# Kernel tuning notes

Hardware: AMD Instinct MI355X
Metric: run time of the kernel (lower is better)

Reference implementation:

```python
import jax, jax.numpy as jnp
import numpy as np

N = 262144            # inflated nodes (atoms + edge-nodes)
E = 4 * 1024 * 1024   # directed edges
D = 8                 # node_feature_dim
TD = 1                # time_dim
H = 32                # hidden_channels
L = 4                 # num_layers
BN_EPS = 1e-5


def setup_inputs() -> dict:
    key = jax.random.key(0)
    ks = jax.random.split(key, 12)
    s = 0.1  # small init scale
    return {
        "x": jax.random.normal(ks[0], (N, D), jnp.float32),
        "t": jax.random.uniform(ks[1], (1,), jnp.float32),
        "edge_index": jax.random.randint(ks[2], (2, E), 0, N, jnp.int32),
        "node_mask": jax.random.randint(ks[3], (N,), 0, 2) > 0,
        "edge_mask": jax.random.randint(ks[4], (N,), 0, 2) > 0,
        "ond": 5,  # original_node_feature_dim
        "oed": 4,  # original_edge_feature_dim
        # GINConv MLP params: layer 0 has in=D+TD, layers 1..3 have in=H
        "W1_first": jax.random.normal(ks[5], (D + TD, H), jnp.float32) * s,
        "b1_first": jnp.zeros((H,), jnp.float32),
        "W2_first": jax.random.normal(ks[6], (H, H), jnp.float32) * s,
        "b2_first": jnp.zeros((H,), jnp.float32),
        "W1_rest": jax.random.normal(ks[7], (L - 1, H, H), jnp.float32) * s,
        "b1_rest": jnp.zeros((L - 1, H), jnp.float32),
        "W2_rest": jax.random.normal(ks[8], (L - 1, H, H), jnp.float32) * s,
        "b2_rest": jnp.zeros((L - 1, H), jnp.float32),
        "eps": jnp.zeros((L,), jnp.float32),           # train_eps=True, init 0
        "bn_gamma": jnp.ones((L, H), jnp.float32),
        "bn_beta": jnp.zeros((L, H), jnp.float32),
        "lin_W": jax.random.normal(ks[9], (L * H, D), jnp.float32) * s,
        "lin_b": jnp.zeros((D,), jnp.float32),
    }


def _gin_forward(x, t, W1_first, b1_first, W2_first, b2_first,
                 W1_rest, b1_rest, W2_rest, b2_rest, eps, bn_gamma, bn_beta,
                 lin_W, lin_b, edge_index, node_mask, edge_mask, ond, oed):
    src = edge_index[0]
    dst = edge_index[1]
    n = x.shape[0]
    # x_in = cat(x, t*ones)
    tcol = jnp.full((n, 1), t[0], x.dtype)
    h = jnp.concatenate([x, tcol], axis=1)  # [N, D+TD]
    xs = []
    for l in range(L):
        # GINConv: (1+eps)*x_i + sum_{j->i} x_j, then 2-layer MLP
        agg = jax.ops.segment_sum(h[src], dst, num_segments=n)  # scatter-add
        z = (1.0 + eps[l]) * h + agg
        W1 = W1_first if l == 0 else W1_rest[l - 1]
        b1 = b1_first if l == 0 else b1_rest[l - 1]
        W2 = W2_first if l == 0 else W2_rest[l - 1]
        b2 = b2_first if l == 0 else b2_rest[l - 1]
        z = jax.nn.relu(z @ W1 + b1) @ W2 + b2  # [N, H]
        # BatchNorm (training-mode batch stats), then ReLU; dropout=eval->id
        mu = jnp.mean(z, axis=0)
        var = jnp.var(z, axis=0)
        z = (z - mu) * jax.lax.rsqrt(var + BN_EPS) * bn_gamma[l] + bn_beta[l]
        h = jax.nn.relu(z)
        xs.append(h)
    # JK 'cat' + final Linear(L*H -> D)
    new_x = jnp.concatenate(xs, axis=1) @ lin_W + lin_b  # [N, D]
    # masked feature write-back: x[mask, 1:dim+1] = new_x[mask, 1:dim+1]
    cols = jnp.arange(x.shape[1])
    ncols = (cols >= 1) & (cols < ond + 1)
    ecols = (cols >= 1) & (cols < oed + 1)
    out = jnp.where(node_mask[:, None] & ncols[None, :], new_x, x)
    out = jnp.where(edge_mask[:, None] & ecols[None, :], new_x, out)
    return out


def reference(x, t, edge_index, node_mask, edge_mask, ond, oed,
              W1_first, b1_first, W2_first, b2_first,
              W1_rest, b1_rest, W2_rest, b2_rest,
              eps, bn_gamma, bn_beta, lin_W, lin_b):
    return _gin_forward(x, t, W1_first, b1_first, W2_first, b2_first,
                        W1_rest, b1_rest, W2_rest, b2_rest,
                        eps, bn_gamma, bn_beta, lin_W, lin_b,
                        edge_index, node_mask, edge_mask, ond, oed)
```

## Files before the change

kernel.cpp:

```cpp
#include <hip/hip_runtime.h>
#include <cstdint>

#define NN 262144
#define EE 4194304
#define CAP 64
#define NB 512
#define BSZ 512
#define NSH 8
#define SCAP 1280
#define EPB 8192
#define SLICES 64

typedef __attribute__((ext_vector_type(8))) short bf16x8;
typedef __attribute__((ext_vector_type(4))) float f32x4;
#define MFMA16 __builtin_amdgcn_mfma_f32_16x16x32_bf16

__device__ inline float bf2f(unsigned short u) {
  union { unsigned int i; float f; } v; v.i = ((unsigned int)u) << 16; return v.f;
}
__device__ inline unsigned short f2bf(float f) {
  union { float f; unsigned int i; } v; v.f = f;
  unsigned int r = v.i + 0x7FFF + ((v.i >> 16) & 1);
  return (unsigned short)(r >> 16);
}
__device__ inline float blo(unsigned int u) {
  union { unsigned int i; float f; } v; v.i = u << 16; return v.f;
}
__device__ inline float bhi(unsigned int u) {
  union { unsigned int i; float f; } v; v.i = u & 0xFFFF0000u; return v.f;
}

__global__ void k_curinit(int* __restrict__ cur) {
  int i = blockIdx.x * 256 + threadIdx.x;
  if (i < NSH * NB) cur[i] = i * SCAP;
}

__global__ void __launch_bounds__(256, 1)
k_bin(const int* __restrict__ ei, int* __restrict__ cur, int* __restrict__ pair) {
  __shared__ int hist[NB];
  __shared__ int off[NB];
  __shared__ int gbase[NB];
  __shared__ int psum[256];
  __shared__ int ebuf[EPB];
  const int tid = threadIdx.x, blk = blockIdx.x, sh = blk & (NSH - 1);
  const int* esrc = ei + (size_t)blk * EPB;
  const int* edst = ei + EE + (size_t)blk * EPB;

  for (int k = tid; k < NB; k += 256) hist[k] = 0;
  __syncthreads();
  for (int j = tid; j < EPB / 4; j += 256) {
    int4 d4 = ((const int4*)edst)[j];
    atomicAdd(&hist[d4.x >> 9], 1);
    atomicAdd(&hist[d4.y >> 9], 1);
    atomicAdd(&hist[d4.z >> 9], 1);
    atomicAdd(&hist[d4.w >> 9], 1);
  }
  __syncthreads();
  int a0 = hist[2 * tid], a1 = hist[2 * tid + 1];
  int ps = a0 + a1;
  psum[tid] = ps;
  __syncthreads();
  for (int d = 1; d < 256; d <<= 1) {
    int v = (tid >= d) ? psum[tid - d] : 0;
    __syncthreads();
    psum[tid] += v;
    __syncthreads();
  }
  int excl = psum[tid] - ps;
  off[2 * tid] = excl;
  off[2 * tid + 1] = excl + a0;
  __syncthreads();
  for (int b = tid; b < NB; b += 256) {
    int n = hist[b];
    int ci = sh * NB + b;
    gbase[b] = n ? atomicAdd(&cur[ci], n) : ci * SCAP;
  }
  __syncthreads();
  for (int k = tid; k < NB; k += 256) hist[k] = off[k];
  __syncthreads();
  for (int j = tid; j < EPB / 4; j += 256) {
    int4 s4 = ((const int4*)esrc)[j];
    int4 d4 = ((const int4*)edst)[j];
    int dd[4] = {d4.x, d4.y, d4.z, d4.w};
    int ss[4] = {s4.x, s4.y, s4.z, s4.w};
#pragma unroll
    for (int u = 0; u < 4; ++u) {
      int bin = dd[u] >> 9, dl = dd[u] & (BSZ - 1);
      int p = atomicAdd(&hist[bin], 1);
      ebuf[p] = ss[u] | (dl << 18);
    }
  }
  __syncthreads();
  for (int b = tid; b < NB; b += 256) {
    int st = off[b];
    int n = hist[b] - st;
    int ci = sh * NB + b;
    int gb = gbase[b];
    int lim = ci * SCAP + SCAP;
    if (gb + n > lim) n = (lim > gb) ? (lim - gb) : 0;
    for (int k = 0; k < n; ++k) pair[gb + k] = ebuf[st + k];
  }
}

__global__ void k_expand(const int* __restrict__ cur, const int* __restrict__ pair,
                         int* __restrict__ slot, int* __restrict__ deg) {
  __shared__ int cbin[BSZ];
  int tid = threadIdx.x;
  int bin = blockIdx.x;
  for (int k = tid; k < BSZ; k += 512) cbin[k] = 0;
  __syncthreads();
  for (int s = 0; s < NSH; ++s) {
    int ci = s * NB + bin, base = ci * SCAP;
    int cnt = min(cur[ci] - base, SCAP);
    for (int k = tid; k < cnt; k += 512) {
      int p = pair[base + k];
      int src = p & 0x3FFFF, dl = p >> 18;
      int pos = atomicAdd(&cbin[dl], 1);
      if (pos < CAP)
        slot[((size_t)bin * BSZ + dl) * CAP + pos] = src;
    }
  }
  __syncthreads();
  for (int k = tid; k < BSZ; k += 512) {
    int cnt = min(cbin[k], CAP);
    int cntp = (cnt + 15) & ~15;
    int self = bin * BSZ + k;
    for (int p = cnt; p < cntp; ++p)
      slot[((size_t)bin * BSZ + k) * CAP + p] = self;
    deg[bin * BSZ + k] = cnt;
  }
}

__global__ void k_layer0(const float* __restrict__ x, const float* __restrict__ t,
                         const int* __restrict__ slot, const int* __restrict__ deg,
                         const float* __restrict__ W1, const float* __restrict__ b1,
                         const float* __restrict__ W2, const float* __restrict__ b2,
                         const float* __restrict__ epsv,
                         unsigned short* __restrict__ zb,
                         float* __restrict__ ssum, float* __restrict__ ssq) {
  __shared__ __align__(16) unsigned short wt1h[32 * 40], wt1l[32 * 40];
  __shared__ __align__(16) unsigned short wt2h[32 * 40], wt2l[32 * 40];
  __shared__ __align__(16) unsigned short insh[16 * 40], insl[16 * 40];
  __shared__ __align__(16) unsigned short z1h[16 * 40], z1l[16 * 40];
  __shared__ float aggs[8][8];
  int tid = threadIdx.x;
  int c = tid & 31, g = tid >> 5;
  size_t base = (size_t)blockIdx.x * 16;

  for (int k = tid; k < 32 * 40; k += 256) { wt1h[k] = 0; wt1l[k] = 0; }
  for (int k = tid; k < 16 * 40; k += 256) { insh[k] = 0; insl[k] = 0; }
  __syncthreads();
  if (tid < 72) {
    float4 wv = ((const float4*)W1)[tid];
    int k = tid >> 3, n4 = (tid & 7) * 4;
    float v[4] = {wv.x, wv.y, wv.z, wv.w};
#pragma unroll
    for (int j = 0; j < 4; ++j) {
      unsigned short h = f2bf(v[j]);
      wt1h[(n4 + j) * 40 + k] = h;
      wt1l[(n4 + j) * 40 + k] = f2bf(v[j] - bf2f(h));
    }
  }
  {
    float4 wv = ((const float4*)W2)[tid];
    int k = tid >> 3, n4 = (tid & 7) * 4;
    float v[4] = {wv.x, wv.y, wv.z, wv.w};
#pragma unroll
    for (int j = 0; j < 4; ++j) {
      unsigned short h = f2bf(v[j]);
      wt2h[(n4 + j) * 40 + k] = h;
      wt2l[(n4 + j) * 40 + k] = f2bf(v[j] - bf2f(h));
    }
  }

  float t0 = t[0];
  float epsl = epsv[0];

  for (int half = 0; half < 2; ++half) {
    int row = g + 8 * half;
    size_t i = base + row;
    int cnt = deg[i];
    int cntp = (cnt + 15) & ~15;
    const int* sl = slot + i * CAP;
    int sv = sl[c];
    float xself = (c < 8) ? x[i * 8 + c] : 0.f;

    int q = c & 1, e = c >> 1;
    float4 agg4 = {0.f, 0.f, 0.f, 0.f};
    int kmax = min(cntp, 32);
    for (int k = 0; k < kmax; k += 16) {
      int s = __shfl(sv, k + e, 32);
      float4 v = ((const float4*)x)[(size_t)s * 2 + q];
      agg4.x += v.x; agg4.y += v.y; agg4.z += v.z; agg4.w += v.w;
    }
    if (cntp > 32) {
      int sv2 = sl[32 + c];
      for (int k = 32; k < cntp; k += 16) {
        int s = __shfl(sv2, (k - 32) + e, 32);
        float4 v = ((const float4*)x)[(size_t)s * 2 + q];
        agg4.x += v.x; agg4.y += v.y; agg4.z += v.z; agg4.w += v.w;
      }
    }
#pragma unroll
    for (int off = 2; off < 32; off <<= 1) {
      agg4.x += __shfl_xor(agg4.x, off, 32);
      agg4.y += __shfl_xor(agg4.y, off, 32);
      agg4.z += __shfl_xor(agg4.z, off, 32);
      agg4.w += __shfl_xor(agg4.w, off, 32);
    }
    if (c < 2) ((float4*)aggs[g])[q] = agg4;
    __syncthreads();

    float pad = (float)(cntp - cnt);
    if (c < 9) {
      float inval = (c < 8) ? ((1.f + epsl) * xself + aggs[g][c] - pad * xself)
                            : ((1.f + epsl) * t0 + (float)cnt * t0);
      unsigned short h = f2bf(inval);
      insh[row * 40 + c] = h;
      insl[row * 40 + c] = f2bf(inval - bf2f(h));
    }
    __syncthreads();
  }

  int w = tid >> 6, lane = tid & 63;
  int nsel = (w & 1) * 16 + (lane & 15);
  int kb = (lane >> 4) * 8;
  if (w < 2) {
    bf16x8 ah = *(const bf16x8*)&insh[(lane & 15) * 40 + kb];
    bf16x8 al = *(const bf16x8*)&insl[(lane & 15) * 40 + kb];
    bf16x8 bh = *(const bf16x8*)&wt1h[nsel * 40 + kb];
    bf16x8 bl = *(const bf16x8*)&wt1l[nsel * 40 + kb];
    f32x4 c1 = {0.f, 0.f, 0.f, 0.f};
    c1 = MFMA16(ah, bh, c1, 0, 0, 0);
    c1 = MFMA16(al, bh, c1, 0, 0, 0);
    c1 = MFMA16(ah, bl, c1, 0, 0, 0);
    float bias1 = b1[nsel];
#pragma unroll
    for (int r = 0; r < 4; ++r) {
      int rr = (lane >> 4) * 4 + r;
      float z = fmaxf(c1[r] + bias1, 0.f);
      unsigned short h = f2bf(z);
      z1h[rr * 40 + nsel] = h;
      z1l[rr * 40 + nsel] = f2bf(z - bf2f(h));
    }
  }
  __syncthreads();
  if (w < 2) {
    bf16x8 ah = *(const bf16x8*)&z1h[(lane & 15) * 40 + kb];
    bf16x8 al = *(const bf16x8*)&z1l[(lane & 15) * 40 + kb];
    bf16x8 bh = *(const bf16x8*)&wt2h[nsel * 40 + kb];
    bf16x8 bl = *(const bf16x8*)&wt2l[nsel * 40 + kb];
    f32x4 c2 = {0.f, 0.f, 0.f, 0.f};
    c2 = MFMA16(ah, bh, c2, 0, 0, 0);
    c2 = MFMA16(al, bh, c2, 0, 0, 0);
    c2 = MFMA16(ah, bl, c2, 0, 0, 0);
    float bias2 = b2[nsel];
    float s1 = 0.f, s2 = 0.f;
#pragma unroll
    for (int r = 0; r < 4; ++r) {
      int rr = (lane >> 4) * 4 + r;
      float z = c2[r] + bias2;
      zb[(base + rr) * 32 + nsel] = f2bf(z);
      s1 += z; s2 += z * z;
    }
    s1 += __shfl_xor(s1, 16, 64); s2 += __shfl_xor(s2, 16, 64);
    s1 += __shfl_xor(s1, 32, 64); s2 += __shfl_xor(s2, 32, 64);
    if ((lane >> 4) == 0) {
      int slice = blockIdx.x & (SLICES - 1);
      atomicAdd(&ssum[slice * 32 + nsel], s1);
      atomicAdd(&ssq[slice * 32 + nsel], s2);
    }
  }
}

__global__ void k_bnapply(const unsigned short* __restrict__ zb,
                          const float* __restrict__ ssum, const float* __restrict__ ssq,
                          const float* __restrict__ gamma, const float* __restrict__ beta,
                          const float* __restrict__ linW,
                          unsigned short* __restrict__ hb,
                          float* __restrict__ out_acc, int first_acc) {
  __shared__ float linWs[256];
  __shared__ float scs[32], shs[32];
  int tid = threadIdx.x;
  for (int k = tid; k < 256; k += 256) linWs[k] = linW[k];
  if (tid < 32) {
    float s1 = 0.f, s2 = 0.f;
    for (int s = 0; s < SLICES; ++s) { s1 += ssum[s * 32 + tid]; s2 += ssq[s * 32 + tid]; }
    float mu = s1 * (1.f / NN);
    float var = s2 * (1.f / NN) - mu * mu;
    float sc = gamma[tid] * rsqrtf(var + 1e-5f);
    scs[tid] = sc;
    shs[tid] = beta[tid] - mu * sc;
  }
  int r = tid & 3;
  size_t n = (size_t)blockIdx.x * 64 + (tid >> 2);
  uint4 u = ((const uint4*)zb)[n * 4 + r];
  __syncthreads();

  float h[8];
#pragma unroll
  for (int j = 0; j < 8; ++j) {
    unsigned int w = (j < 2) ? u.x : (j < 4) ? u.y : (j < 6) ? u.z : u.w;
    float zv = (j & 1) ? bhi(w) : blo(w);
    h[j] = fmaxf(zv * scs[8 * r + j] + shs[8 * r + j], 0.f);
  }
  uint4 o;
  o.x = (unsigned int)f2bf(h[0]) | ((unsigned int)f2bf(h[1]) << 16);
  o.y = (unsigned int)f2bf(h[2]) | ((unsigned int)f2bf(h[3]) << 16);
  o.z = (unsigned int)f2bf(h[4]) | ((unsigned int)f2bf(h[5]) << 16);
  o.w = (unsigned int)f2bf(h[6]) | ((unsigned int)f2bf(h[7]) << 16);
  ((uint4*)hb)[n * 4 + r] = o;

  float jk[8];
#pragma unroll
  for (int d = 0; d < 8; ++d) {
    float a = 0.f;
#pragma unroll
    for (int j = 0; j < 8; ++j) a += h[j] * linWs[(8 * r + j) * 8 + d];
    jk[d] = a;
  }
#pragma unroll
  for (int off = 1; off <= 2; off <<= 1)
#pragma unroll
    for (int d = 0; d < 8; ++d) jk[d] += __shfl_xor(jk[d], off, 64);
  if (r == 0) {
    float4 a0 = {jk[0], jk[1], jk[2], jk[3]};
    float4 a1 = {jk[4], jk[5], jk[6], jk[7]};
    if (!first_acc) {
      float4 p0 = ((const float4*)out_acc)[n * 2];
      float4 p1 = ((const float4*)out_acc)[n * 2 + 1];
      a0.x += p0.x; a0.y += p0.y; a0.z += p0.z; a0.w += p0.w;
      a1.x += p1.x; a1.y += p1.y; a1.z += p1.z; a1.w += p1.w;
    }
    ((float4*)out_acc)[n * 2] = a0;
    ((float4*)out_acc)[n * 2 + 1] = a1;
  }
}

__global__ void k_layerN(const unsigned short* __restrict__ hb,
                         const int* __restrict__ slot, const int* __restrict__ deg,
                         const float* __restrict__ W1, const float* __restrict__ b1,
                         const float* __restrict__ W2, const float* __restrict__ b2,
                         const float* __restrict__ epsv, int l,
                         unsigned short* __restrict__ zbo,
                         float* __restrict__ ssum, float* __restrict__ ssq) {
  __shared__ __align__(16) unsigned short wt1h[32 * 40], wt1l[32 * 40];
  __shared__ __align__(16) unsigned short wt2h[32 * 40], wt2l[32 * 40];
  __shared__ __align__(16) unsigned short insh[16 * 40], insl[16 * 40];
  __shared__ __align__(16) unsigned short z1h[16 * 40], z1l[16 * 40];
  __shared__ float aggs[8][32];
  int tid = threadIdx.x;
  int c = tid & 31, g = tid >> 5;
  size_t base = (size_t)blockIdx.x * 16;

  {
    float4 w1v = ((const float4*)W1)[tid];
    float4 w2v = ((const float4*)W2)[tid];
    int k = tid >> 3, n4 = (tid & 7) * 4;
    float v1[4] = {w1v.x, w1v.y, w1v.z, w1v.w};
    float v2[4] = {w2v.x, w2v.y, w2v.z, w2v.w};
#pragma unroll
    for (int j = 0; j < 4; ++j) {
      unsigned short h1 = f2bf(v1[j]);
      wt1h[(n4 + j) * 40 + k] = h1;
      wt1l[(n4 + j) * 40 + k] = f2bf(v1[j] - bf2f(h1));
      unsigned short h2 = f2bf(v2[j]);
      wt2h[(n4 + j) * 40 + k] = h2;
      wt2l[(n4 + j) * 40 + k] = f2bf(v2[j] - bf2f(h2));
    }
  }

  float epsl = epsv[l];

  for (int half = 0; half < 2; ++half) {
    int row = g + 8 * half;
    size_t i = base + row;
    int cnt = deg[i];
    int cntp = (cnt + 15) & ~15;
    const int* sl = slot + i * CAP;
    int sv = sl[c];
    float hself = bf2f(hb[i * 32 + c]);

    int q = c & 7, sub = c >> 3;
    const ushort4* h4 = (const ushort4*)hb;
    float4 agg4 = {0.f, 0.f, 0.f, 0.f};
    int kmax = min(cntp, 32);
    for (int k = 0; k < kmax; k += 16) {
      int sa = __shfl(sv, k + sub, 32);
      int sb = __shfl(sv, k + 4 + sub, 32);
      int sc_ = __shfl(sv, k + 8 + sub, 32);
      int sd = __shfl(sv, k + 12 + sub, 32);
      ushort4 ua = h4[(size_t)sa * 8 + q];
      ushort4 ub = h4[(size_t)sb * 8 + q];
      ushort4 uc = h4[(size_t)sc_ * 8 + q];
      ushort4 ud = h4[(size_t)sd * 8 + q];
      agg4.x += bf2f(ua.x) + bf2f(ub.x) + bf2f(uc.x) + bf2f(ud.x);
      agg4.y += bf2f(ua.y) + bf2f(ub.y) + bf2f(uc.y) + bf2f(ud.y);
      agg4.z += bf2f(ua.z) + bf2f(ub.z) + bf2f(uc.z) + bf2f(ud.z);
      agg4.w += bf2f(ua.w) + bf2f(ub.w) + bf2f(uc.w) + bf2f(ud.w);
    }
    if (cntp > 32) {
      int sv2 = sl[32 + c];
      for (int k = 32; k < cntp; k += 16) {
        int kk = k - 32;
        int sa = __shfl(sv2, kk + sub, 32);
        int sb = __shfl(sv2, kk + 4 + sub, 32);
        int sc_ = __shfl(sv2, kk + 8 + sub, 32);
        int sd = __shfl(sv2, kk + 12 + sub, 32);
        ushort4 ua = h4[(size_t)sa * 8 + q];
        ushort4 ub = h4[(size_t)sb * 8 + q];
        ushort4 uc = h4[(size_t)sc_ * 8 + q];
        ushort4 ud = h4[(size_t)sd * 8 + q];
        agg4.x += bf2f(ua.x) + bf2f(ub.x) + bf2f(uc.x) + bf2f(ud.x);
        agg4.y += bf2f(ua.y) + bf2f(ub.y) + bf2f(uc.y) + bf2f(ud.y);
        agg4.z += bf2f(ua.z) + bf2f(ub.z) + bf2f(uc.z) + bf2f(ud.z);
        agg4.w += bf2f(ua.w) + bf2f(ub.w) + bf2f(uc.w) + bf2f(ud.w);
      }
    }
    agg4.x += __shfl_xor(agg4.x, 8, 32);
    agg4.y += __shfl_xor(agg4.y, 8, 32);
    agg4.z += __shfl_xor(agg4.z, 8, 32);
    agg4.w += __shfl_xor(agg4.w, 8, 32);
    agg4.x += __shfl_xor(agg4.x, 16, 32);
    agg4.y += __shfl_xor(agg4.y, 16, 32);
    agg4.z += __shfl_xor(agg4.z, 16, 32);
    agg4.w += __shfl_xor(agg4.w, 16, 32);
    if (c < 8) ((float4*)aggs[g])[q] = agg4;
    __syncthreads();

    float pad = (float)(cntp - cnt);
    float inval = (1.f + epsl - pad) * hself + aggs[g][c];
    unsigned short h = f2bf(inval);
    insh[row * 40 + c] = h;
    insl[row * 40 + c] = f2bf(inval - bf2f(h));
    __syncthreads();
  }

  int w = tid >> 6, lane = tid & 63;
  int nsel = (w & 1) * 16 + (lane & 15);
  int kb = (lane >> 4) * 8;
  if (w < 2) {
    bf16x8 ah = *(const bf16x8*)&insh[(lane & 15) * 40 + kb];
    bf16x8 al = *(const bf16x8*)&insl[(lane & 15) * 40 + kb];
    bf16x8 bh = *(const bf16x8*)&wt1h[nsel * 40 + kb];
    bf16x8 bl = *(const bf16x8*)&wt1l[nsel * 40 + kb];
    f32x4 c1 = {0.f, 0.f, 0.f, 0.f};
    c1 = MFMA16(ah, bh, c1, 0, 0, 0);
    c1 = MFMA16(al, bh, c1, 0, 0, 0);
    c1 = MFMA16(ah, bl, c1, 0, 0, 0);
    float bias1 = b1[nsel];
#pragma unroll
    for (int r = 0; r < 4; ++r) {
      int rr = (lane >> 4) * 4 + r;
      float z = fmaxf(c1[r] + bias1, 0.f);
      unsigned short h = f2bf(z);
      z1h[rr * 40 + nsel] = h;
      z1l[rr * 40 + nsel] = f2bf(z - bf2f(h));
    }
  }
  __syncthreads();
  if (w < 2) {
    bf16x8 ah = *(const bf16x8*)&z1h[(lane & 15) * 40 + kb];
    bf16x8 al = *(const bf16x8*)&z1l[(lane & 15) * 40 + kb];
    bf16x8 bh = *(const bf16x8*)&wt2h[nsel * 40 + kb];
    bf16x8 bl = *(const bf16x8*)&wt2l[nsel * 40 + kb];
    f32x4 c2 = {0.f, 0.f, 0.f, 0.f};
    c2 = MFMA16(ah, bh, c2, 0, 0, 0);
    c2 = MFMA16(al, bh, c2, 0, 0, 0);
    c2 = MFMA16(ah, bl, c2, 0, 0, 0);
    float bias2 = b2[nsel];
    float s1 = 0.f, s2 = 0.f;
#pragma unroll
    for (int r = 0; r < 4; ++r) {
      int rr = (lane >> 4) * 4 + r;
      float z = c2[r] + bias2;
      zbo[(base + rr) * 32 + nsel] = f2bf(z);
      s1 += z; s2 += z * z;
    }
    s1 += __shfl_xor(s1, 16, 64); s2 += __shfl_xor(s2, 16, 64);
    s1 += __shfl_xor(s1, 32, 64); s2 += __shfl_xor(s2, 32, 64);
    if ((lane >> 4) == 0) {
      int slice = blockIdx.x & (SLICES - 1);
      atomicAdd(&ssum[slice * 32 + nsel], s1);
      atomicAdd(&ssq[slice * 32 + nsel], s2);
    }
  }
}

__global__ void k_final(const unsigned short* __restrict__ z3,
                        const float* __restrict__ ssum, const float* __restrict__ ssq,
                        const float* __restrict__ gamma, const float* __restrict__ beta,
                        const float* __restrict__ linW3, const float* __restrict__ lin_b,
                        const float* __restrict__ out_acc, const float* __restrict__ x,
                        const int* __restrict__ nm, const int* __restrict__ em,
                        const int* __restrict__ ondp, const int* __restrict__ oedp,
                        float* __restrict__ out) {
  __shared__ float linWs[256];
  __shared__ float scs[32], shs[32];
  int tid = threadIdx.x;
  for (int k = tid; k < 256; k += 256) linWs[k] = linW3[k];
  if (tid < 32) {
    float s1 = 0.f, s2 = 0.f;
    for (int s = 0; s < SLICES; ++s) { s1 += ssum[s * 32 + tid]; s2 += ssq[s * 32 + tid]; }
    float mu = s1 * (1.f / NN);
    float var = s2 * (1.f / NN) - mu * mu;
    float sc = gamma[tid] * rsqrtf(var + 1e-5f);
    scs[tid] = sc;
    shs[tid] = beta[tid] - mu * sc;
  }
  int r = tid & 3;
  size_t n = (size_t)blockIdx.x * 64 + (tid >> 2);
  uint4 u = ((const uint4*)z3)[n * 4 + r];
  __syncthreads();

  float h[8];
#pragma unroll
  for (int j = 0; j < 8; ++j) {
    unsigned int w = (j < 2) ? u.x : (j < 4) ? u.y : (j < 6) ? u.z : u.w;
    float zv = (j & 1) ? bhi(w) : blo(w);
    h[j] = fmaxf(zv * scs[8 * r + j] + shs[8 * r + j], 0.f);
  }
  float jk[8];
#pragma unroll
  for (int d = 0; d < 8; ++d) {
    float a = 0.f;
#pragma unroll
    for (int j = 0; j < 8; ++j) a += h[j] * linWs[(8 * r + j) * 8 + d];
    jk[d] = a;
  }
#pragma unroll
  for (int off = 1; off <= 2; off <<= 1)
#pragma unroll
    for (int d = 0; d < 8; ++d) jk[d] += __shfl_xor(jk[d], off, 64);
  if (r == 0) {
    float4 p0 = ((const float4*)out_acc)[n * 2];
    float4 p1 = ((const float4*)out_acc)[n * 2 + 1];
    float4 x0 = ((const float4*)x)[n * 2];
    float4 x1 = ((const float4*)x)[n * 2 + 1];
    float res[8] = {jk[0] + p0.x + lin_b[0], jk[1] + p0.y + lin_b[1],
                    jk[2] + p0.z + lin_b[2], jk[3] + p0.w + lin_b[3],
                    jk[4] + p1.x + lin_b[4], jk[5] + p1.y + lin_b[5],
                    jk[6] + p1.z + lin_b[6], jk[7] + p1.w + lin_b[7]};
    float xs[8] = {x0.x, x0.y, x0.z, x0.w, x1.x, x1.y, x1.z, x1.w};
    int ond = ondp[0], oed = oedp[0];
    bool nmv = nm[n] != 0, emv = em[n] != 0;
    float o[8];
#pragma unroll
    for (int d = 0; d < 8; ++d) {
      bool w = (d >= 1) && ((nmv && d < ond + 1) || (emv && d < oed + 1));
      o[d] = w ? res[d] : xs[d];
    }
    ((float4*)out)[n * 2]     = make_float4(o[0], o[1], o[2], o[3]);
    ((float4*)out)[n * 2 + 1] = make_float4(o[4], o[5], o[6], o[7]);
  }
}

extern "C" void kernel_launch(void* const* d_in, const int* in_sizes, int n_in,
                              void* d_out, int out_size, void* d_ws, size_t ws_size,
                              hipStream_t stream) {
  const float* x        = (const float*)d_in[0];
  const float* t        = (const float*)d_in[1];
  const int*   ei       = (const int*)d_in[2];
  const int*   node_mask= (const int*)d_in[3];
  const int*   edge_mask= (const int*)d_in[4];
  const int*   ondp     = (const int*)d_in[5];
  const int*   oedp     = (const int*)d_in[6];
  const float* W1_first = (const float*)d_in[7];
  const float* b1_first = (const float*)d_in[8];
  const float* W2_first = (const float*)d_in[9];
  const float* b2_first = (const float*)d_in[10];
  const float* W1_rest  = (const float*)d_in[11];
  const float* b1_rest  = (const float*)d_in[12];
  const float* W2_rest  = (const float*)d_in[13];
  const float* b2_rest  = (const float*)d_in[14];
  const float* epsv     = (const float*)d_in[15];
  const float* bn_gamma = (const float*)d_in[16];
  const float* bn_beta  = (const float*)d_in[17];
  const float* lin_W    = (const float*)d_in[18];
  const float* lin_b    = (const float*)d_in[19];
  float* out = (float*)d_out;

  char* ws = (char*)d_ws;
  size_t off = 0;
  int*   slot    = (int*)(ws + off);   off += (size_t)NN * CAP * 4;
  int*   pair    = (int*)(ws + off);   off += (size_t)NSH * NB * SCAP * 4;
  int*   cur     = (int*)(ws + off);   off += (size_t)NSH * NB * 4;
  int*   deg     = (int*)(ws + off);   off += (size_t)NN * 4;
  unsigned short* zb = (unsigned short*)(ws + off); off += (size_t)NN * 32 * 2;
  unsigned short* hb = (unsigned short*)(ws + off); off += (size_t)NN * 32 * 2;
  float* out_acc = (float*)(ws + off); off += (size_t)NN * 8 * 4;
  float* stats   = (float*)(ws + off); off += (size_t)4 * 2 * SLICES * 32 * 4;
  (void)ws_size; (void)in_sizes; (void)n_in; (void)out_size;

  hipMemsetAsync(stats, 0, (size_t)4 * 2 * SLICES * 32 * 4, stream);
  k_curinit<<<(NSH * NB + 255) / 256, 256, 0, stream>>>(cur);
  k_bin<<<EE / EPB, 256, 0, stream>>>(ei, cur, pair);
  k_expand<<<NB, 512, 0, stream>>>(cur, pair, slot, deg);

  {
    float* ssum = stats;
    float* ssq  = ssum + SLICES * 32;
    k_layer0<<<NN / 16, 256, 0, stream>>>(x, t, slot, deg, W1_first, b1_first,
                                          W2_first, b2_first, epsv, zb, ssum, ssq);
    k_bnapply<<<NN / 64, 256, 0, stream>>>(zb, ssum, ssq, bn_gamma, bn_beta,
                                           lin_W, hb, out_acc, 1);
  }
  for (int l = 1; l < 4; ++l) {
    const float* W1 = W1_rest + (size_t)(l - 1) * 32 * 32;
    const float* b1 = b1_rest + (size_t)(l - 1) * 32;
    const float* W2 = W2_rest + (size_t)(l - 1) * 32 * 32;
    const float* b2 = b2_rest + (size_t)(l - 1) * 32;
    float* ssum = stats + (size_t)l * 2 * SLICES * 32;
    float* ssq  = ssum + SLICES * 32;
    k_layerN<<<NN / 16, 256, 0, stream>>>(hb, slot, deg, W1, b1, W2, b2,
                                          epsv, l, zb, ssum, ssq);
    if (l < 3)
      k_bnapply<<<NN / 64, 256, 0, stream>>>(zb, ssum, ssq, bn_gamma + l * 32,
                                             bn_beta + l * 32,
                                             lin_W + (size_t)l * 32 * 8,
                                             hb, out_acc, 0);
  }
  k_final<<<NN / 64, 256, 0, stream>>>(zb, stats + 3 * 2 * SLICES * 32,
                                       stats + 3 * 2 * SLICES * 32 + SLICES * 32,
                                       bn_gamma + 96, bn_beta + 96,
                                       lin_W + 3 * 32 * 8, lin_b, out_acc, x,
                                       node_mask, edge_mask, ondp, oedp, out);
}
```

Measured before the change: 523.0 us.

## Precompute swizzled split-bf16 weight images, pad neighbors to 8, interleave two-row gathers

```diff
diff --git a/kernel.cpp b/kernel.cpp
--- a/kernel.cpp
+++ b/kernel.cpp
@@ -13,6 +13,7 @@
 
 typedef __attribute__((ext_vector_type(8))) short bf16x8;
 typedef __attribute__((ext_vector_type(4))) float f32x4;
+typedef __attribute__((ext_vector_type(2))) float f32x2;
 #define MFMA16 __builtin_amdgcn_mfma_f32_16x16x32_bf16
 
 __device__ inline float bf2f(unsigned short u) {
@@ -29,10 +30,46 @@
 __device__ inline float bhi(unsigned int u) {
   union { unsigned int i; float f; } v; v.i = u & 0xFFFF0000u; return v.f;
 }
-
-__global__ void k_curinit(int* __restrict__ cur) {
-  int i = blockIdx.x * 256 + threadIdx.x;
-  if (i < NSH * NB) cur[i] = i * SCAP;
+__device__ inline f32x2 bfpair(unsigned int u) {
+  union { unsigned int i; float f; } lo, hi;
+  lo.i = u << 16; hi.i = u & 0xFFFF0000u;
+  return (f32x2){lo.f, hi.f};
+}
+
+__global__ void k_prep(int* __restrict__ cur,
+                       const float* __restrict__ W1f, const float* __restrict__ W2f,
+                       const float* __restrict__ W1r, const float* __restrict__ W2r,
+                       unsigned short* __restrict__ wimg) {
+  int tid = threadIdx.x;
+  if (blockIdx.x < 16) {
+    int i = blockIdx.x * 256 + tid;
+    if (i < NSH * NB) cur[i] = i * SCAP;
+    return;
+  }
+  for (int k = tid; k < 4 * 4 * 1280; k += 256) wimg[k] = 0;
+  __syncthreads();
+  for (int l = 0; l < 4; ++l) {
+    const float* W1 = (l == 0) ? W1f : W1r + (size_t)(l - 1) * 1024;
+    const float* W2 = (l == 0) ? W2f : W2r + (size_t)(l - 1) * 1024;
+    int kdim = (l == 0) ? 9 : 32;
+    unsigned short* bm = wimg + (size_t)l * 5120;
+    for (int e = tid; e < kdim * 32; e += 256) {
+      int k = e >> 5, n = e & 31;
+      float v = W1[e];
+      unsigned short h = f2bf(v);
+      int idx = n * 40 + (k ^ (n & 8));
+      bm[idx] = h;
+      bm[1280 + idx] = f2bf(v - bf2f(h));
+    }
+    for (int e = tid; e < 1024; e += 256) {
+      int k = e >> 5, n = e & 31;
+      float v = W2[e];
+      unsigned short h = f2bf(v);
+      int idx = n * 40 + (k ^ (n & 8));
+      bm[2560 + idx] = h;
+      bm[3840 + idx] = f2bf(v - bf2f(h));
+    }
+  }
 }
 
 __global__ void __launch_bounds__(256, 1)
@@ -123,7 +160,7 @@
   __syncthreads();
   for (int k = tid; k < BSZ; k += 512) {
     int cnt = min(cbin[k], CAP);
-    int cntp = (cnt + 15) & ~15;
+    int cntp = (cnt + 7) & ~7;
     int self = bin * BSZ + k;
     for (int p = cnt; p < cntp; ++p)
       slot[((size_t)bin * BSZ + k) * CAP + p] = self;
@@ -133,103 +170,112 @@
 
 __global__ void k_layer0(const float* __restrict__ x, const float* __restrict__ t,
                          const int* __restrict__ slot, const int* __restrict__ deg,
-                         const float* __restrict__ W1, const float* __restrict__ b1,
-                         const float* __restrict__ W2, const float* __restrict__ b2,
+                         const unsigned short* __restrict__ wimg,
+                         const float* __restrict__ b1, const float* __restrict__ b2,
                          const float* __restrict__ epsv,
                          unsigned short* __restrict__ zb,
                          float* __restrict__ ssum, float* __restrict__ ssq) {
-  __shared__ __align__(16) unsigned short wt1h[32 * 40], wt1l[32 * 40];
-  __shared__ __align__(16) unsigned short wt2h[32 * 40], wt2l[32 * 40];
-  __shared__ __align__(16) unsigned short insh[16 * 40], insl[16 * 40];
-  __shared__ __align__(16) unsigned short z1h[16 * 40], z1l[16 * 40];
-  __shared__ float aggs[8][8];
+  __shared__ __align__(16) unsigned short wbuf[5120];
+  __shared__ __align__(16) unsigned short insh[640], insl[640], z1h[640], z1l[640];
+  __shared__ float aggs0[2][8][8];
   int tid = threadIdx.x;
   int c = tid & 31, g = tid >> 5;
   size_t base = (size_t)blockIdx.x * 16;
 
-  for (int k = tid; k < 32 * 40; k += 256) { wt1h[k] = 0; wt1l[k] = 0; }
-  for (int k = tid; k < 16 * 40; k += 256) { insh[k] = 0; insl[k] = 0; }
-  __syncthreads();
-  if (tid < 72) {
-    float4 wv = ((const float4*)W1)[tid];
-    int k = tid >> 3, n4 = (tid & 7) * 4;
-    float v[4] = {wv.x, wv.y, wv.z, wv.w};
-#pragma unroll
-    for (int j = 0; j < 4; ++j) {
-      unsigned short h = f2bf(v[j]);
-      wt1h[(n4 + j) * 40 + k] = h;
-      wt1l[(n4 + j) * 40 + k] = f2bf(v[j] - bf2f(h));
-    }
-  }
   {
-    float4 wv = ((const float4*)W2)[tid];
-    int k = tid >> 3, n4 = (tid & 7) * 4;
-    float v[4] = {wv.x, wv.y, wv.z, wv.w};
-#pragma unroll
-    for (int j = 0; j < 4; ++j) {
-      unsigned short h = f2bf(v[j]);
-      wt2h[(n4 + j) * 40 + k] = h;
-      wt2l[(n4 + j) * 40 + k] = f2bf(v[j] - bf2f(h));
-    }
-  }
+    const uint4* srcw = (const uint4*)wimg;
+    uint4* dstw = (uint4*)wbuf;
+    for (int k = tid; k < 640; k += 256) dstw[k] = srcw[k];
+  }
+  for (int k = tid; k < 640; k += 256) { insh[k] = 0; insl[k] = 0; }
 
   float t0 = t[0];
   float epsl = epsv[0];
-
-  for (int half = 0; half < 2; ++half) {
-    int row = g + 8 * half;
-    size_t i = base + row;
-    int cnt = deg[i];
-    int cntp = (cnt + 15) & ~15;
-    const int* sl = slot + i * CAP;
-    int sv = sl[c];
-    float xself = (c < 8) ? x[i * 8 + c] : 0.f;
-
-    int q = c & 1, e = c >> 1;
-    float4 agg4 = {0.f, 0.f, 0.f, 0.f};
-    int kmax = min(cntp, 32);
-    for (int k = 0; k < kmax; k += 16) {
-      int s = __shfl(sv, k + e, 32);
-      float4 v = ((const float4*)x)[(size_t)s * 2 + q];
-      agg4.x += v.x; agg4.y += v.y; agg4.z += v.z; agg4.w += v.w;
-    }
-    if (cntp > 32) {
-      int sv2 = sl[32 + c];
-      for (int k = 32; k < cntp; k += 16) {
-        int s = __shfl(sv2, (k - 32) + e, 32);
-        float4 v = ((const float4*)x)[(size_t)s * 2 + q];
-        agg4.x += v.x; agg4.y += v.y; agg4.z += v.z; agg4.w += v.w;
-      }
-    }
-#pragma unroll
-    for (int off = 2; off < 32; off <<= 1) {
-      agg4.x += __shfl_xor(agg4.x, off, 32);
-      agg4.y += __shfl_xor(agg4.y, off, 32);
-      agg4.z += __shfl_xor(agg4.z, off, 32);
-      agg4.w += __shfl_xor(agg4.w, off, 32);
-    }
-    if (c < 2) ((float4*)aggs[g])[q] = agg4;
-    __syncthreads();
-
-    float pad = (float)(cntp - cnt);
-    if (c < 9) {
-      float inval = (c < 8) ? ((1.f + epsl) * xself + aggs[g][c] - pad * xself)
-                            : ((1.f + epsl) * t0 + (float)cnt * t0);
-      unsigned short h = f2bf(inval);
-      insh[row * 40 + c] = h;
-      insl[row * 40 + c] = f2bf(inval - bf2f(h));
-    }
-    __syncthreads();
-  }
+  size_t i0 = base + g, i1 = base + g + 8;
+  int cnt0 = deg[i0], cnt1 = deg[i1];
+  int cntp0 = (cnt0 + 7) & ~7, cntp1 = (cnt1 + 7) & ~7;
+  const int* sl0 = slot + i0 * CAP;
+  const int* sl1 = slot + i1 * CAP;
+  int sv0 = sl0[c], sv1 = sl1[c];
+  float xs0 = (c < 8) ? x[i0 * 8 + c] : 0.f;
+  float xs1 = (c < 8) ? x[i1 * 8 + c] : 0.f;
+
+  int q = c & 3, sub = c >> 2;
+  const float2* x2 = (const float2*)x;
+  f32x2 ac0 = {0.f, 0.f}, ac1 = {0.f, 0.f};
+  int km0 = min(cntp0, 32), km1 = min(cntp1, 32);
+  int kb_ = min(km0, km1);
+  for (int k = 0; k < kb_; k += 8) {
+    int s0 = __shfl(sv0, k + sub, 32);
+    int s1 = __shfl(sv1, k + sub, 32);
+    float2 v0 = x2[(size_t)s0 * 4 + q];
+    float2 v1 = x2[(size_t)s1 * 4 + q];
+    ac0 += (f32x2){v0.x, v0.y};
+    ac1 += (f32x2){v1.x, v1.y};
+  }
+  for (int k = kb_; k < km0; k += 8) {
+    int s0 = __shfl(sv0, k + sub, 32);
+    float2 v0 = x2[(size_t)s0 * 4 + q];
+    ac0 += (f32x2){v0.x, v0.y};
+  }
+  for (int k = kb_; k < km1; k += 8) {
+    int s1 = __shfl(sv1, k + sub, 32);
+    float2 v1 = x2[(size_t)s1 * 4 + q];
+    ac1 += (f32x2){v1.x, v1.y};
+  }
+  if (cntp0 > 32) {
+    int sv2 = sl0[32 + c];
+    for (int k = 32; k < cntp0; k += 8) {
+      int s0 = __shfl(sv2, k - 32 + sub, 32);
+      float2 v0 = x2[(size_t)s0 * 4 + q];
+      ac0 += (f32x2){v0.x, v0.y};
+    }
+  }
+  if (cntp1 > 32) {
+    int sv2 = sl1[32 + c];
+    for (int k = 32; k < cntp1; k += 8) {
+      int s1 = __shfl(sv2, k - 32 + sub, 32);
+      float2 v1 = x2[(size_t)s1 * 4 + q];
+      ac1 += (f32x2){v1.x, v1.y};
+    }
+  }
+#pragma unroll
+  for (int off = 4; off < 32; off <<= 1) {
+    ac0.x += __shfl_xor(ac0.x, off, 32);
+    ac0.y += __shfl_xor(ac0.y, off, 32);
+    ac1.x += __shfl_xor(ac1.x, off, 32);
+    ac1.y += __shfl_xor(ac1.y, off, 32);
+  }
+  if (c < 4) {
+    aggs0[0][g][2 * c] = ac0.x; aggs0[0][g][2 * c + 1] = ac0.y;
+    aggs0[1][g][2 * c] = ac1.x; aggs0[1][g][2 * c + 1] = ac1.y;
+  }
+  __syncthreads();
+  if (c < 9) {
+    float p0 = (float)(cntp0 - cnt0), p1 = (float)(cntp1 - cnt1);
+    float inv0 = (c < 8) ? ((1.f + epsl) * xs0 + aggs0[0][g][c] - p0 * xs0)
+                         : ((1.f + epsl) * t0 + (float)cnt0 * t0);
+    float inv1 = (c < 8) ? ((1.f + epsl) * xs1 + aggs0[1][g][c] - p1 * xs1)
+                         : ((1.f + epsl) * t0 + (float)cnt1 * t0);
+    int ii0 = g * 40 + c;
+    int ii1 = (g + 8) * 40 + (c ^ 8);
+    unsigned short h0 = f2bf(inv0), h1 = f2bf(inv1);
+    insh[ii0] = h0; insl[ii0] = f2bf(inv0 - bf2f(h0));
+    insh[ii1] = h1; insl[ii1] = f2bf(inv1 - bf2f(h1));
+  }
+  __syncthreads();
 
   int w = tid >> 6, lane = tid & 63;
-  int nsel = (w & 1) * 16 + (lane & 15);
-  int kb = (lane >> 4) * 8;
+  int m = lane & 15, gk = lane >> 4;
+  int nsel = (w & 1) * 16 + m;
+  int kb = gk * 8;
+  int aoff = m * 40 + (kb ^ (m & 8));
+  int boff = nsel * 40 + (kb ^ (m & 8));
   if (w < 2) {
-    bf16x8 ah = *(const bf16x8*)&insh[(lane & 15) * 40 + kb];
-    bf16x8 al = *(const bf16x8*)&insl[(lane & 15) * 40 + kb];
-    bf16x8 bh = *(const bf16x8*)&wt1h[nsel * 40 + kb];
-    bf16x8 bl = *(const bf16x8*)&wt1l[nsel * 40 + kb];
+    bf16x8 ah = *(const bf16x8*)&insh[aoff];
+    bf16x8 al = *(const bf16x8*)&insl[aoff];
+    bf16x8 bh = *(const bf16x8*)&wbuf[boff];
+    bf16x8 bl = *(const bf16x8*)&wbuf[1280 + boff];
     f32x4 c1 = {0.f, 0.f, 0.f, 0.f};
     c1 = MFMA16(ah, bh, c1, 0, 0, 0);
     c1 = MFMA16(al, bh, c1, 0, 0, 0);
@@ -237,19 +283,20 @@
     float bias1 = b1[nsel];
 #pragma unroll
     for (int r = 0; r < 4; ++r) {
-      int rr = (lane >> 4) * 4 + r;
+      int rr = gk * 4 + r;
       float z = fmaxf(c1[r] + bias1, 0.f);
       unsigned short h = f2bf(z);
-      z1h[rr * 40 + nsel] = h;
-      z1l[rr * 40 + nsel] = f2bf(z - bf2f(h));
+      int zi = rr * 40 + (nsel ^ (rr & 8));
+      z1h[zi] = h;
+      z1l[zi] = f2bf(z - bf2f(h));
     }
   }
   __syncthreads();
   if (w < 2) {
-    bf16x8 ah = *(const bf16x8*)&z1h[(lane & 15) * 40 + kb];
-    bf16x8 al = *(const bf16x8*)&z1l[(lane & 15) * 40 + kb];
-    bf16x8 bh = *(const bf16x8*)&wt2h[nsel * 40 + kb];
-    bf16x8 bl = *(const bf16x8*)&wt2l[nsel * 40 + kb];
+    bf16x8 ah = *(const bf16x8*)&z1h[aoff];
+    bf16x8 al = *(const bf16x8*)&z1l[aoff];
+    bf16x8 bh = *(const bf16x8*)&wbuf[2560 + boff];
+    bf16x8 bl = *(const bf16x8*)&wbuf[3840 + boff];
     f32x4 c2 = {0.f, 0.f, 0.f, 0.f};
     c2 = MFMA16(ah, bh, c2, 0, 0, 0);
     c2 = MFMA16(al, bh, c2, 0, 0, 0);
@@ -258,14 +305,14 @@
     float s1 = 0.f, s2 = 0.f;
 #pragma unroll
     for (int r = 0; r < 4; ++r) {
-      int rr = (lane >> 4) * 4 + r;
+      int rr = gk * 4 + r;
       float z = c2[r] + bias2;
       zb[(base + rr) * 32 + nsel] = f2bf(z);
       s1 += z; s2 += z * z;
     }
     s1 += __shfl_xor(s1, 16, 64); s2 += __shfl_xor(s2, 16, 64);
     s1 += __shfl_xor(s1, 32, 64); s2 += __shfl_xor(s2, 32, 64);
-    if ((lane >> 4) == 0) {
+    if (gk == 0) {
       int slice = blockIdx.x & (SLICES - 1);
       atomicAdd(&ssum[slice * 32 + nsel], s1);
       atomicAdd(&ssq[slice * 32 + nsel], s2);
@@ -339,111 +386,119 @@
 
 __global__ void k_layerN(const unsigned short* __restrict__ hb,
                          const int* __restrict__ slot, const int* __restrict__ deg,
-                         const float* __restrict__ W1, const float* __restrict__ b1,
-                         const float* __restrict__ W2, const float* __restrict__ b2,
+                         const unsigned short* __restrict__ wimg,
+                         const float* __restrict__ b1, const float* __restrict__ b2,
                          const float* __restrict__ epsv, int l,
                          unsigned short* __restrict__ zbo,
                          float* __restrict__ ssum, float* __restrict__ ssq) {
-  __shared__ __align__(16) unsigned short wt1h[32 * 40], wt1l[32 * 40];
-  __shared__ __align__(16) unsigned short wt2h[32 * 40], wt2l[32 * 40];
-  __shared__ __align__(16) unsigned short insh[16 * 40], insl[16 * 40];
-  __shared__ __align__(16) unsigned short z1h[16 * 40], z1l[16 * 40];
-  __shared__ float aggs[8][32];
+  __shared__ __align__(16) unsigned short wbuf[5120];
+  __shared__ __align__(16) unsigned short insh[640], insl[640], z1h[640], z1l[640];
+  __shared__ __align__(16) float aggs[2][8][4][36];
   int tid = threadIdx.x;
   int c = tid & 31, g = tid >> 5;
   size_t base = (size_t)blockIdx.x * 16;
 
   {
-    float4 w1v = ((const float4*)W1)[tid];
-    float4 w2v = ((const float4*)W2)[tid];
-    int k = tid >> 3, n4 = (tid & 7) * 4;
-    float v1[4] = {w1v.x, w1v.y, w1v.z, w1v.w};
-    float v2[4] = {w2v.x, w2v.y, w2v.z, w2v.w};
-#pragma unroll
-    for (int j = 0; j < 4; ++j) {
-      unsigned short h1 = f2bf(v1[j]);
-      wt1h[(n4 + j) * 40 + k] = h1;
-      wt1l[(n4 + j) * 40 + k] = f2bf(v1[j] - bf2f(h1));
-      unsigned short h2 = f2bf(v2[j]);
-      wt2h[(n4 + j) * 40 + k] = h2;
-      wt2l[(n4 + j) * 40 + k] = f2bf(v2[j] - bf2f(h2));
-    }
+    const uint4* srcw = (const uint4*)(wimg + (size_t)l * 5120);
+    uint4* dstw = (uint4*)wbuf;
+    for (int k = tid; k < 640; k += 256) dstw[k] = srcw[k];
   }
 
   float epsl = epsv[l];
-
-  for (int half = 0; half < 2; ++half) {
-    int row = g + 8 * half;
-    size_t i = base + row;
-    int cnt = deg[i];
-    int cntp = (cnt + 15) & ~15;
-    const int* sl = slot + i * CAP;
-    int sv = sl[c];
-    float hself = bf2f(hb[i * 32 + c]);
-
-    int q = c & 7, sub = c >> 3;
-    const ushort4* h4 = (const ushort4*)hb;
-    float4 agg4 = {0.f, 0.f, 0.f, 0.f};
-    int kmax = min(cntp, 32);
-    for (int k = 0; k < kmax; k += 16) {
-      int sa = __shfl(sv, k + sub, 32);
-      int sb = __shfl(sv, k + 4 + sub, 32);
-      int sc_ = __shfl(sv, k + 8 + sub, 32);
-      int sd = __shfl(sv, k + 12 + sub, 32);
-      ushort4 ua = h4[(size_t)sa * 8 + q];
-      ushort4 ub = h4[(size_t)sb * 8 + q];
-      ushort4 uc = h4[(size_t)sc_ * 8 + q];
-      ushort4 ud = h4[(size_t)sd * 8 + q];
-      agg4.x += bf2f(ua.x) + bf2f(ub.x) + bf2f(uc.x) + bf2f(ud.x);
-      agg4.y += bf2f(ua.y) + bf2f(ub.y) + bf2f(uc.y) + bf2f(ud.y);
-      agg4.z += bf2f(ua.z) + bf2f(ub.z) + bf2f(uc.z) + bf2f(ud.z);
-      agg4.w += bf2f(ua.w) + bf2f(ub.w) + bf2f(uc.w) + bf2f(ud.w);
-    }
-    if (cntp > 32) {
-      int sv2 = sl[32 + c];
-      for (int k = 32; k < cntp; k += 16) {
-        int kk = k - 32;
-        int sa = __shfl(sv2, kk + sub, 32);
-        int sb = __shfl(sv2, kk + 4 + sub, 32);
-        int sc_ = __shfl(sv2, kk + 8 + sub, 32);
-        int sd = __shfl(sv2, kk + 12 + sub, 32);
-        ushort4 ua = h4[(size_t)sa * 8 + q];
-        ushort4 ub = h4[(size_t)sb * 8 + q];
-        ushort4 uc = h4[(size_t)sc_ * 8 + q];
-        ushort4 ud = h4[(size_t)sd * 8 + q];
-        agg4.x += bf2f(ua.x) + bf2f(ub.x) + bf2f(uc.x) + bf2f(ud.x);
-        agg4.y += bf2f(ua.y) + bf2f(ub.y) + bf2f(uc.y) + bf2f(ud.y);
-        agg4.z += bf2f(ua.z) + bf2f(ub.z) + bf2f(uc.z) + bf2f(ud.z);
-        agg4.w += bf2f(ua.w) + bf2f(ub.w) + bf2f(uc.w) + bf2f(ud.w);
-      }
-    }
-    agg4.x += __shfl_xor(agg4.x, 8, 32);
-    agg4.y += __shfl_xor(agg4.y, 8, 32);
-    agg4.z += __shfl_xor(agg4.z, 8, 32);
-    agg4.w += __shfl_xor(agg4.w, 8, 32);
-    agg4.x += __shfl_xor(agg4.x, 16, 32);
-    agg4.y += __shfl_xor(agg4.y, 16, 32);
-    agg4.z += __shfl_xor(agg4.z, 16, 32);
-    agg4.w += __shfl_xor(agg4.w, 16, 32);
-    if (c < 8) ((float4*)aggs[g])[q] = agg4;
-    __syncthreads();
-
-    float pad = (float)(cntp - cnt);
-    float inval = (1.f + epsl - pad) * hself + aggs[g][c];
-    unsigned short h = f2bf(inval);
-    insh[row * 40 + c] = h;
-    insl[row * 40 + c] = f2bf(inval - bf2f(h));
-    __syncthreads();
-  }
+  size_t i0 = base + g, i1 = base + g + 8;
+  int cnt0 = deg[i0], cnt1 = deg[i1];
+  int cntp0 = (cnt0 + 7) & ~7, cntp1 = (cnt1 + 7) & ~7;
+  const int* sl0 = slot + i0 * CAP;
+  const int* sl1 = slot + i1 * CAP;
+  int sv0 = sl0[c], sv1 = sl1[c];
+  float hs0 = bf2f(hb[i0 * 32 + c]);
+  float hs1 = bf2f(hb[i1 * 32 + c]);
+
+  int q = c & 7, sub = c >> 3;
+  const uint2* h2 = (const uint2*)hb;
+  f32x2 a001 = {0.f, 0.f}, a023 = {0.f, 0.f};
+  f32x2 a101 = {0.f, 0.f}, a123 = {0.f, 0.f};
+  int km0 = min(cntp0, 32), km1 = min(cntp1, 32);
+  int kb_ = min(km0, km1);
+  for (int k = 0; k < kb_; k += 8) {
+    int sa0 = __shfl(sv0, k + sub, 32);
+    int sb0 = __shfl(sv0, k + 4 + sub, 32);
+    int sa1 = __shfl(sv1, k + sub, 32);
+    int sb1 = __shfl(sv1, k + 4 + sub, 32);
+    uint2 ua = h2[(size_t)sa0 * 8 + q];
+    uint2 ub = h2[(size_t)sb0 * 8 + q];
+    uint2 uc = h2[(size_t)sa1 * 8 + q];
+    uint2 ud = h2[(size_t)sb1 * 8 + q];
+    a001 += bfpair(ua.x); a023 += bfpair(ua.y);
+    a001 += bfpair(ub.x); a023 += bfpair(ub.y);
+    a101 += bfpair(uc.x); a123 += bfpair(uc.y);
+    a101 += bfpair(ud.x); a123 += bfpair(ud.y);
+  }
+  for (int k = kb_; k < km0; k += 8) {
+    int sa0 = __shfl(sv0, k + sub, 32);
+    int sb0 = __shfl(sv0, k + 4 + sub, 32);
+    uint2 ua = h2[(size_t)sa0 * 8 + q];
+    uint2 ub = h2[(size_t)sb0 * 8 + q];
+    a001 += bfpair(ua.x); a023 += bfpair(ua.y);
+    a001 += bfpair(ub.x); a023 += bfpair(ub.y);
+  }
+  for (int k = kb_; k < km1; k += 8) {
+    int sa1 = __shfl(sv1, k + sub, 32);
+    int sb1 = __shfl(sv1, k + 4 + sub, 32);
+    uint2 uc = h2[(size_t)sa1 * 8 + q];
+    uint2 ud = h2[(size_t)sb1 * 8 + q];
+    a101 += bfpair(uc.x); a123 += bfpair(uc.y);
+    a101 += bfpair(ud.x); a123 += bfpair(ud.y);
+  }
+  if (cntp0 > 32) {
+    int sv2 = sl0[32 + c];
+    for (int k = 32; k < cntp0; k += 8) {
+      int sa0 = __shfl(sv2, k - 32 + sub, 32);
+      int sb0 = __shfl(sv2, k - 28 + sub, 32);
+      uint2 ua = h2[(size_t)sa0 * 8 + q];
+      uint2 ub = h2[(size_t)sb0 * 8 + q];
+      a001 += bfpair(ua.x); a023 += bfpair(ua.y);
+      a001 += bfpair(ub.x); a023 += bfpair(ub.y);
+    }
+  }
+  if (cntp1 > 32) {
+    int sv2 = sl1[32 + c];
+    for (int k = 32; k < cntp1; k += 8) {
+      int sa1 = __shfl(sv2, k - 32 + sub, 32);
+      int sb1 = __shfl(sv2, k - 28 + sub, 32);
+      uint2 uc = h2[(size_t)sa1 * 8 + q];
+      uint2 ud = h2[(size_t)sb1 * 8 + q];
+      a101 += bfpair(uc.x); a123 += bfpair(uc.y);
+      a101 += bfpair(ud.x); a123 += bfpair(ud.y);
+    }
+  }
+  *(float4*)&aggs[0][g][sub][q * 4] = make_float4(a001.x, a001.y, a023.x, a023.y);
+  *(float4*)&aggs[1][g][sub][q * 4] = make_float4(a101.x, a101.y, a123.x, a123.y);
+  __syncthreads();
+  {
+    float s0 = aggs[0][g][0][c] + aggs[0][g][1][c] + aggs[0][g][2][c] + aggs[0][g][3][c];
+    float s1 = aggs[1][g][0][c] + aggs[1][g][1][c] + aggs[1][g][2][c] + aggs[1][g][3][c];
+    float inv0 = (1.f + epsl - (float)(cntp0 - cnt0)) * hs0 + s0;
+    float inv1 = (1.f + epsl - (float)(cntp1 - cnt1)) * hs1 + s1;
+    int ii0 = g * 40 + c;
+    int ii1 = (g + 8) * 40 + (c ^ 8);
+    unsigned short h0 = f2bf(inv0), h1 = f2bf(inv1);
+    insh[ii0] = h0; insl[ii0] = f2bf(inv0 - bf2f(h0));
+    insh[ii1] = h1; insl[ii1] = f2bf(inv1 - bf2f(h1));
+  }
+  __syncthreads();
 
   int w = tid >> 6, lane = tid & 63;
-  int nsel = (w & 1) * 16 + (lane & 15);
-  int kb = (lane >> 4) * 8;
+  int m = lane & 15, gk = lane >> 4;
+  int nsel = (w & 1) * 16 + m;
+  int kb = gk * 8;
+  int aoff = m * 40 + (kb ^ (m & 8));
+  int boff = nsel * 40 + (kb ^ (m & 8));
   if (w < 2) {
-    bf16x8 ah = *(const bf16x8*)&insh[(lane & 15) * 40 + kb];
-    bf16x8 al = *(const bf16x8*)&insl[(lane & 15) * 40 + kb];
-    bf16x8 bh = *(const bf16x8*)&wt1h[nsel * 40 + kb];
-    bf16x8 bl = *(const bf16x8*)&wt1l[nsel * 40 + kb];
+    bf16x8 ah = *(const bf16x8*)&insh[aoff];
+    bf16x8 al = *(const bf16x8*)&insl[aoff];
+    bf16x8 bh = *(const bf16x8*)&wbuf[boff];
+    bf16x8 bl = *(const bf16x8*)&wbuf[1280 + boff];
     f32x4 c1 = {0.f, 0.f, 0.f, 0.f};
     c1 = MFMA16(ah, bh, c1, 0, 0, 0);
     c1 = MFMA16(al, bh, c1, 0, 0, 0);
@@ -451,19 +506,20 @@
     float bias1 = b1[nsel];
 #pragma unroll
     for (int r = 0; r < 4; ++r) {
-      int rr = (lane >> 4) * 4 + r;
+      int rr = gk * 4 + r;
       float z = fmaxf(c1[r] + bias1, 0.f);
       unsigned short h = f2bf(z);
-      z1h[rr * 40 + nsel] = h;
-      z1l[rr * 40 + nsel] = f2bf(z - bf2f(h));
+      int zi = rr * 40 + (nsel ^ (rr & 8));
+      z1h[zi] = h;
+      z1l[zi] = f2bf(z - bf2f(h));
     }
   }
   __syncthreads();
   if (w < 2) {
-    bf16x8 ah = *(const bf16x8*)&z1h[(lane & 15) * 40 + kb];
-    bf16x8 al = *(const bf16x8*)&z1l[(lane & 15) * 40 + kb];
-    bf16x8 bh = *(const bf16x8*)&wt2h[nsel * 40 + kb];
-    bf16x8 bl = *(const bf16x8*)&wt2l[nsel * 40 + kb];
+    bf16x8 ah = *(const bf16x8*)&z1h[aoff];
+    bf16x8 al = *(const bf16x8*)&z1l[aoff];
+    bf16x8 bh = *(const bf16x8*)&wbuf[2560 + boff];
+    bf16x8 bl = *(const bf16x8*)&wbuf[3840 + boff];
     f32x4 c2 = {0.f, 0.f, 0.f, 0.f};
     c2 = MFMA16(ah, bh, c2, 0, 0, 0);
     c2 = MFMA16(al, bh, c2, 0, 0, 0);
@@ -472,14 +528,14 @@
     float s1 = 0.f, s2 = 0.f;
 #pragma unroll
     for (int r = 0; r < 4; ++r) {
-      int rr = (lane >> 4) * 4 + r;
+      int rr = gk * 4 + r;
       float z = c2[r] + bias2;
       zbo[(base + rr) * 32 + nsel] = f2bf(z);
       s1 += z; s2 += z * z;
     }
     s1 += __shfl_xor(s1, 16, 64); s2 += __shfl_xor(s2, 16, 64);
     s1 += __shfl_xor(s1, 32, 64); s2 += __shfl_xor(s2, 32, 64);
-    if ((lane >> 4) == 0) {
+    if (gk == 0) {
       int slice = blockIdx.x & (SLICES - 1);
       atomicAdd(&ssum[slice * 32 + nsel], s1);
       atomicAdd(&ssq[slice * 32 + nsel], s2);
@@ -590,29 +646,28 @@
   unsigned short* hb = (unsigned short*)(ws + off); off += (size_t)NN * 32 * 2;
   float* out_acc = (float*)(ws + off); off += (size_t)NN * 8 * 4;
   float* stats   = (float*)(ws + off); off += (size_t)4 * 2 * SLICES * 32 * 4;
+  unsigned short* wimg = (unsigned short*)(ws + off); off += (size_t)4 * 4 * 1280 * 2;
   (void)ws_size; (void)in_sizes; (void)n_in; (void)out_size;
 
   hipMemsetAsync(stats, 0, (size_t)4 * 2 * SLICES * 32 * 4, stream);
-  k_curinit<<<(NSH * NB + 255) / 256, 256, 0, stream>>>(cur);
+  k_prep<<<17, 256, 0, stream>>>(cur, W1_first, W2_first, W1_rest, W2_rest, wimg);
   k_bin<<<EE / EPB, 256, 0, stream>>>(ei, cur, pair);
   k_expand<<<NB, 512, 0, stream>>>(cur, pair, slot, deg);
 
   {
     float* ssum = stats;
     float* ssq  = ssum + SLICES * 32;
-    k_layer0<<<NN / 16, 256, 0, stream>>>(x, t, slot, deg, W1_first, b1_first,
-                                          W2_first, b2_first, epsv, zb, ssum, ssq);
+    k_layer0<<<NN / 16, 256, 0, stream>>>(x, t, slot, deg, wimg, b1_first,
+                                          b2_first, epsv, zb, ssum, ssq);
     k_bnapply<<<NN / 64, 256, 0, stream>>>(zb, ssum, ssq, bn_gamma, bn_beta,
                                            lin_W, hb, out_acc, 1);
   }
   for (int l = 1; l < 4; ++l) {
-    const float* W1 = W1_rest + (size_t)(l - 1) * 32 * 32;
     const float* b1 = b1_rest + (size_t)(l - 1) * 32;
-    const float* W2 = W2_rest + (size_t)(l - 1) * 32 * 32;
     const float* b2 = b2_rest + (size_t)(l - 1) * 32;
     float* ssum = stats + (size_t)l * 2 * SLICES * 32;
     float* ssq  = ssum + SLICES * 32;
-    k_layerN<<<NN / 16, 256, 0, stream>>>(hb, slot, deg, W1, b1, W2, b2,
+    k_layerN<<<NN / 16, 256, 0, stream>>>(hb, slot, deg, wimg, b1, b2,
                                           epsv, l, zb, ssum, ssq);
     if (l < 3)
       k_bnapply<<<NN / 64, 256, 0, stream>>>(zb, ssum, ssq, bn_gamma + l * 32,
```

After: 529.3 us. About the same (+1.2%).
